# Performance work log

Measured on AMD Instinct MI355X. Metric: run time of the kernel, lower is better.

Reference implementation:

```python
import jax, jax.numpy as jnp
import numpy as np

T, B, NINP, NHID = 1024, 64, 2048, 2048


def setup_inputs() -> dict:
    key = jax.random.key(0)
    ks = jax.random.split(key, 10)
    s = 0.02  # small init for numerical sanity (torch code used uniform(0,1))
    return {
        "x": jax.random.normal(ks[0], (T, B, NINP), dtype=jnp.float32),
        "hidden": jax.random.normal(ks[1], (B, NHID), dtype=jnp.float32),
        "W_cx": jax.random.normal(ks[2], (NHID, NINP), dtype=jnp.float32) * s,
        "W_ih": jax.random.normal(ks[3], (NHID, NHID), dtype=jnp.float32) * s,
        "W_ix": jax.random.normal(ks[4], (NHID, NINP), dtype=jnp.float32) * s,
        "W_fh": jax.random.normal(ks[5], (NHID, NHID), dtype=jnp.float32) * s,
        "W_fx": jax.random.normal(ks[6], (NHID, NINP), dtype=jnp.float32) * s,
        "b_i": jnp.zeros((NHID,), dtype=jnp.float32),
        "b_f": jnp.zeros((NHID,), dtype=jnp.float32),
    }


def reference(x, hidden, W_cx, W_ih, W_ix, W_fh, W_fx, b_i, b_f):
    # Precompute all input-side projections in big batched GEMMs (same math,
    # hoisted out of the sequential loop).
    content = jnp.einsum('tbi,hi->tbh', x, W_cx)            # [T,B,H]
    ix = jnp.einsum('tbi,hi->tbh', x, W_ix) + b_i            # [T,B,H]
    fx = jnp.einsum('tbi,hi->tbh', x, W_fx) + b_f            # [T,B,H]

    def step(h, inp):
        c_t, ix_t, fx_t = inp
        i_t = jax.nn.sigmoid(h @ W_ih.T + ix_t)
        f_t = jax.nn.sigmoid(h @ W_fh.T + fx_t)
        h_new = jnp.tanh(i_t * c_t + f_t * h)
        return h_new, h_new

    nexth, output = jax.lax.scan(step, hidden, (content, ix, fx))
    return output, nexth
```

## Files before the change

### kernel.cpp

```cpp
#include <hip/hip_runtime.h>
#include <cstdint>
#include <cstddef>

#define T_SEQ 1024
#define BATCH 64
#define NH 2048

typedef _Float16 half8 __attribute__((ext_vector_type(8)));
typedef _Float16 half4 __attribute__((ext_vector_type(4)));
typedef float f32x4 __attribute__((ext_vector_type(4)));
typedef unsigned u32x4 __attribute__((ext_vector_type(4)));

__device__ inline void gload_lds16(const void* g, void* l) {
    __builtin_amdgcn_global_load_lds(
        (const __attribute__((address_space(1))) uint32_t*)g,
        (__attribute__((address_space(3))) uint32_t*)l,
        16, 0, 0);
}

#define LLC_LD16NW(dst, addr)                                                \
    asm volatile("global_load_dwordx4 %0, %1, off sc0 sc1"                   \
                 : "=v"(dst) : "v"(addr))
#define LLC_LD4(dst, addr)                                                   \
    asm volatile("global_load_dword %0, %1, off sc0 sc1\n\ts_waitcnt vmcnt(0)" \
                 : "=v"(dst) : "v"(addr))
#define LLC_LD16W(dst, addr)                                                 \
    asm volatile("global_load_dwordx4 %0, %1, off sc0 sc1\n\ts_waitcnt vmcnt(0)" \
                 : "=v"(dst) : "v"(addr))
#define LLC_ST2(addr, val)                                                   \
    asm volatile("global_store_short %0, %1, off sc0 sc1"                    \
                 :: "v"(addr), "v"(val) : "memory")
#define LLC_ST4(addr, val)                                                   \
    asm volatile("global_store_dword %0, %1, off sc0 sc1"                    \
                 :: "v"(addr), "v"(val) : "memory")
#define LLC_ST16(addr, val)                                                  \
    asm volatile("global_store_dwordx4 %0, %1, off sc0 sc1"                  \
                 :: "v"(addr), "v"(val) : "memory")

__device__ inline void wait_vm0() {
    asm volatile("s_waitcnt vmcnt(0)" ::: "memory");
}

__global__ __launch_bounds__(256) void cvt_f32_f16(const float* __restrict__ src,
                                                   _Float16* __restrict__ dst,
                                                   long long n) {
    long long i = ((long long)blockIdx.x * 256 + threadIdx.x) * 4;
    long long stride = (long long)gridDim.x * 256 * 4;
    for (; i < n; i += stride) {
        const float4 v = *(const float4*)(src + i);
        half4 o;
        o[0] = (_Float16)v.x; o[1] = (_Float16)v.y;
        o[2] = (_Float16)v.z; o[3] = (_Float16)v.w;
        *(half4*)(dst + i) = o;
    }
}

__global__ __launch_bounds__(256) void proj_gemm(const _Float16* __restrict__ A,
                                                 const _Float16* __restrict__ B,
                                                 _Float16* __restrict__ C, int M) {
    __shared__ _Float16 As[128][64];
    __shared__ _Float16 Bs[128][64];
    const int NBN = 48;
    const int nbm = M >> 7;
    const int nwg = nbm * NBN;
    const int per = nwg >> 3;
    const int bid = blockIdx.x;
    const int swz = (bid & 7) * per + (bid >> 3);
    const int bm = swz / NBN, bn = swz % NBN;

    const int tid = threadIdx.x;
    const int lane = tid & 63, w = tid >> 6;
    const int wm = w & 1, wn = w >> 1;

    f32x4 acc[4][4] = {};

    const int srow = lane >> 3;
    const int scol = (lane & 7) * 8;

    for (int bk = 0; bk < NH / 64; ++bk) {
#pragma unroll
        for (int i = 0; i < 4; ++i) {
            int r = w * 32 + i * 8;
            const _Float16* gA = A + (size_t)(bm * 128 + r + srow) * NH + bk * 64 + scol;
            gload_lds16(gA, &As[r][0]);
            const _Float16* gB = B + (size_t)(bn * 128 + r + srow) * NH + bk * 64 + scol;
            gload_lds16(gB, &Bs[r][0]);
        }
        __syncthreads();
#pragma unroll
        for (int kk = 0; kk < 2; ++kk) {
            half8 af[4], bf[4];
#pragma unroll
            for (int mi = 0; mi < 4; ++mi)
                af[mi] = *(const half8*)&As[wm * 64 + mi * 16 + (lane & 15)][kk * 32 + (lane >> 4) * 8];
#pragma unroll
            for (int ni = 0; ni < 4; ++ni)
                bf[ni] = *(const half8*)&Bs[wn * 64 + ni * 16 + (lane & 15)][kk * 32 + (lane >> 4) * 8];
#pragma unroll
            for (int mi = 0; mi < 4; ++mi)
#pragma unroll
                for (int ni = 0; ni < 4; ++ni)
                    acc[mi][ni] = __builtin_amdgcn_mfma_f32_16x16x32_f16(af[mi], bf[ni], acc[mi][ni], 0, 0, 0);
        }
        __syncthreads();
    }
#pragma unroll
    for (int mi = 0; mi < 4; ++mi)
#pragma unroll
        for (int ni = 0; ni < 4; ++ni)
#pragma unroll
            for (int r = 0; r < 4; ++r) {
                int m = bm * 128 + wm * 64 + mi * 16 + (lane >> 4) * 4 + r;
                int n = bn * 128 + wn * 64 + ni * 16 + (lane & 15);
                C[(size_t)m * 6144 + n] = (_Float16)acc[mi][ni][r];
            }
}

__global__ __launch_bounds__(512, 1) void scan_kernel(
    const _Float16* __restrict__ proj,
    const _Float16* __restrict__ Wr,
    _Float16* hb0, _Float16* hb1,
    const float* __restrict__ b_i, const float* __restrict__ b_f,
    float* __restrict__ out,
    unsigned* hflags, unsigned* pflags, float* part,
    int t0, int nsteps) {
    extern __shared__ char smem[];
    _Float16* Wlds = (_Float16*)smem;
    char* hstage = smem + 131072;

    const int wg = blockIdx.x;
    const int xcd = wg & 7;
    const int slot = wg >> 3;
    const int g = slot & 1;
    const int rem = slot >> 1;
    const int js = xcd * 4 + (rem & 3);
    const int ks = rem >> 2;
    const int j0g = js * 64;
    const int b0 = g * 32;
    const int k0 = ks * 512;

    const int tid = threadIdx.x;
    const int lane = tid & 63;
    const int w = tid >> 6;
    const int mi = w & 1;
    const int nt = w >> 1;

    unsigned* hflags_g = hflags + g * 32;
    unsigned* pflags_g = pflags + g * 128;

    for (int q = 0; q < 16; ++q) {
        int e = q * 512 + tid;
        int le = e & 63;
        int u = (e >> 6) & 15;
        int nte = (e >> 10) & 3;
        int gate = e >> 12;
        const _Float16* src = Wr + ((size_t)gate << 22) +
            (size_t)(j0g + nte * 16 + (le & 15)) * NH + k0 + u * 32 + (le >> 4) * 8;
        *(half8*)(Wlds + (((size_t)(gate * 4 + nte) * 16 + u) * 64 + le) * 8) =
            *(const half8*)src;
    }

    const int jj = j0g + nt * 16 + (lane & 15);
    const float bi_s = b_i[jj];
    const float bf_s = b_f[jj];

    float hprev[4], pc[4], pix[4], pfx[4];
    if (ks == 0) {
        const _Float16* hini = (t0 & 1) ? hb1 : hb0;
#pragma unroll
        for (int r = 0; r < 4; ++r) {
            int b = b0 + mi * 16 + (lane >> 4) * 4 + r;
            unsigned tmp;
            asm volatile("global_load_ushort %0, %1, off sc0 sc1\n\ts_waitcnt vmcnt(0)"
                         : "=v"(tmp) : "v"(hini + (size_t)b * NH + jj));
            hprev[r] = (float)__builtin_bit_cast(_Float16, (unsigned short)tmp);
            size_t pbase = (size_t)b * 6144 + jj;
            pc[r] = (float)proj[pbase];
            pix[r] = (float)proj[pbase + 2048];
            pfx[r] = (float)proj[pbase + 4096];
        }
    }

    __syncthreads();

    for (int s = 0; s < nsteps; ++s) {
        const int t = t0 + s;
        const _Float16* hcur = (t & 1) ? hb1 : hb0;
        _Float16* hnxt = (t & 1) ? hb0 : hb1;
        const unsigned tv = (unsigned)t;

        if (w == 0) {
            const unsigned* fa = hflags_g + ks * 8 + (lane & 7);
            while (true) {
                unsigned v;
                LLC_LD4(v, fa);
                if (__all((int)(v >= tv))) break;
                __builtin_amdgcn_s_sleep(1);
            }
        }
        __syncthreads();

        {
            half8 t0v, t1v, t2v, t3v;
            const _Float16* srcb = hcur + (size_t)(b0 + w * 4) * NH + k0 + lane * 8;
            LLC_LD16NW(t0v, srcb);
            LLC_LD16NW(t1v, srcb + NH);
            LLC_LD16NW(t2v, srcb + 2 * NH);
            LLC_LD16NW(t3v, srcb + 3 * NH);
            wait_vm0();
            __builtin_amdgcn_sched_barrier(0);
            const int r0 = w * 4;
            *(half8*)(hstage + (r0 + 0) * 1024 + ((lane * 16) ^ (((r0 + 0) & 7) << 4))) = t0v;
            *(half8*)(hstage + (r0 + 1) * 1024 + ((lane * 16) ^ (((r0 + 1) & 7) << 4))) = t1v;
            *(half8*)(hstage + (r0 + 2) * 1024 + ((lane * 16) ^ (((r0 + 2) & 7) << 4))) = t2v;
            *(half8*)(hstage + (r0 + 3) * 1024 + ((lane * 16) ^ (((r0 + 3) & 7) << 4))) = t3v;
        }
        __syncthreads();

        f32x4 ci = {}, cf = {};
        {
            const int arow = mi * 16 + (lane & 15);
            const char* abase = hstage + arow * 1024;
            const int axor = (arow & 7) << 4;
            const _Float16* wbi = Wlds + (((size_t)(0 * 4 + nt) * 16) * 64 + lane) * 8;
            const _Float16* wbf = Wlds + (((size_t)(1 * 4 + nt) * 16) * 64 + lane) * 8;
#pragma unroll
            for (int u = 0; u < 16; ++u) {
                half8 a = *(const half8*)(abase + ((u * 64 + (lane >> 4) * 16) ^ axor));
                half8 wi = *(const half8*)(wbi + (size_t)u * 512);
                half8 wf = *(const half8*)(wbf + (size_t)u * 512);
                ci = __builtin_amdgcn_mfma_f32_16x16x32_f16(a, wi, ci, 0, 0, 0);
                cf = __builtin_amdgcn_mfma_f32_16x16x32_f16(a, wf, cf, 0, 0, 0);
            }
        }

        if (ks != 0) {
            const int slotp = (((t & 1) * 2 + g) * 32 + js) * 3 + (ks - 1);
            float* pb = part + (size_t)slotp * 4096 + w * 512 + lane * 4;
            LLC_ST16(pb, ci);
            LLC_ST16(pb + 256, cf);
            wait_vm0();
            __syncthreads();
            if (tid == 0) LLC_ST4(pflags_g + js * 4 + (ks - 1), (unsigned)(t + 1));
        } else {
            if (w == 0) {
                const unsigned* pf = pflags_g + js * 4;
                while (true) {
                    u32x4 v;
                    LLC_LD16W(v, pf);
                    if (__all((int)(v[0] >= tv + 1 && v[1] >= tv + 1 && v[2] >= tv + 1)))
                        break;
                    __builtin_amdgcn_s_sleep(1);
                }
            }
            __syncthreads();

            f32x4 pi0, pg0, pi1, pg1, pi2, pg2;
            const int sbase = (((t & 1) * 2 + g) * 32 + js) * 3;
            const float* pb0 = part + (size_t)(sbase + 0) * 4096 + w * 512 + lane * 4;
            const float* pb1 = part + (size_t)(sbase + 1) * 4096 + w * 512 + lane * 4;
            const float* pb2 = part + (size_t)(sbase + 2) * 4096 + w * 512 + lane * 4;
            LLC_LD16NW(pi0, pb0);
            LLC_LD16NW(pg0, pb0 + 256);
            LLC_LD16NW(pi1, pb1);
            LLC_LD16NW(pg1, pb1 + 256);
            LLC_LD16NW(pi2, pb2);
            LLC_LD16NW(pg2, pb2 + 256);
            wait_vm0();
            __builtin_amdgcn_sched_barrier(0);
            ci += pi0 + pi1 + pi2;
            cf += pg0 + pg1 + pg2;

            float hn_keep[4];
#pragma unroll
            for (int r = 0; r < 4; ++r) {
                int b = b0 + mi * 16 + (lane >> 4) * 4 + r;
                float iv = 1.0f / (1.0f + __expf(-(ci[r] + pix[r] + bi_s)));
                float fv = 1.0f / (1.0f + __expf(-(cf[r] + pfx[r] + bf_s)));
                float z = iv * pc[r] + fv * hprev[r];
                float hn = 1.0f - 2.0f / (__expf(2.0f * z) + 1.0f);
                hprev[r] = hn;
                hn_keep[r] = hn;
                _Float16 hn16 = (_Float16)hn;
                LLC_ST2(hnxt + (size_t)b * NH + jj, hn16);
            }
            wait_vm0();
            __syncthreads();
            if (tid == 0) LLC_ST4(hflags_g + js, (unsigned)(t + 1));

#pragma unroll
            for (int r = 0; r < 4; ++r) {
                int b = b0 + mi * 16 + (lane >> 4) * 4 + r;
                out[(size_t)t * (BATCH * NH) + (size_t)b * NH + jj] = hn_keep[r];
                if (t == T_SEQ - 1)
                    out[(size_t)T_SEQ * (BATCH * NH) + (size_t)b * NH + jj] = hn_keep[r];
            }
            if (s + 1 < nsteps) {
#pragma unroll
                for (int r = 0; r < 4; ++r) {
                    int b = b0 + mi * 16 + (lane >> 4) * 4 + r;
                    size_t pbase = ((size_t)(s + 1) * 64 + b) * 6144 + jj;
                    pc[r] = (float)proj[pbase];
                    pix[r] = (float)proj[pbase + 2048];
                    pfx[r] = (float)proj[pbase + 4096];
                }
            }
        }
    }
}

extern "C" void kernel_launch(void* const* d_in, const int* in_sizes, int n_in,
                              void* d_out, int out_size, void* d_ws, size_t ws_size,
                              hipStream_t stream) {
    const float* x = (const float*)d_in[0];
    const float* hidden = (const float*)d_in[1];
    const float* W_cx = (const float*)d_in[2];
    const float* W_ih = (const float*)d_in[3];
    const float* W_ix = (const float*)d_in[4];
    const float* W_fh = (const float*)d_in[5];
    const float* W_fx = (const float*)d_in[6];
    const float* b_i = (const float*)d_in[7];
    const float* b_f = (const float*)d_in[8];
    float* out = (float*)d_out;

    char* ws = (char*)d_ws;
    size_t off = 0;
    auto alloc = [&](size_t bytes) {
        char* p = ws + off;
        off += (bytes + 255) & ~(size_t)255;
        return p;
    };
    _Float16* Wp = (_Float16*)alloc((size_t)6144 * NH * 2);
    _Float16* Wr = (_Float16*)alloc((size_t)2 * NH * NH * 2);
    _Float16* hb0 = (_Float16*)alloc((size_t)BATCH * NH * 2);
    _Float16* hb1 = (_Float16*)alloc((size_t)BATCH * NH * 2);
    unsigned* hflags = (unsigned*)alloc(256);
    unsigned* pflags = (unsigned*)alloc(1024);
    float* part = (float*)alloc((size_t)2 * 2 * 32 * 3 * 4096 * 4);
    const size_t fixed = off;

    int chunk = 32;
    for (int c = T_SEQ; c >= 32; c >>= 1) {
        size_t need = fixed + (size_t)c * 64 * NH * 2 + (size_t)c * 64 * 6144 * 2 + 1024;
        if (need <= ws_size) { chunk = c; break; }
    }
    _Float16* xh = (_Float16*)alloc((size_t)chunk * 64 * NH * 2);
    _Float16* proj = (_Float16*)alloc((size_t)chunk * 64 * 6144 * 2);

    hipMemsetAsync(hflags, 0, 256, stream);
    hipMemsetAsync(pflags, 0, 1024, stream);

    const long long wsz = (long long)NH * NH;
    cvt_f32_f16<<<2048, 256, 0, stream>>>(W_cx, Wp, wsz);
    cvt_f32_f16<<<2048, 256, 0, stream>>>(W_ix, Wp + wsz, wsz);
    cvt_f32_f16<<<2048, 256, 0, stream>>>(W_fx, Wp + 2 * wsz, wsz);
    cvt_f32_f16<<<2048, 256, 0, stream>>>(W_ih, Wr, wsz);
    cvt_f32_f16<<<2048, 256, 0, stream>>>(W_fh, Wr + wsz, wsz);
    cvt_f32_f16<<<128, 256, 0, stream>>>(hidden, hb0, (long long)BATCH * NH);

    const int nch = T_SEQ / chunk;
    for (int c = 0; c < nch; ++c) {
        const int t0 = c * chunk;
        const int M = chunk * 64;
        cvt_f32_f16<<<2048, 256, 0, stream>>>(x + (size_t)t0 * 64 * NH, xh, (long long)M * NH);
        proj_gemm<<<dim3((M / 128) * 48), 256, 0, stream>>>(xh, Wp, proj, M);
        scan_kernel<<<256, 512, 163840, stream>>>(proj, Wr, hb0, hb1, b_i, b_f,
                                                  out, hflags, pflags, part, t0, chunk);
    }
}
```

Measured before the change: 9.895 ms.

## Replace partial-sum flags with canary-tagged fp16 partials polled directly

The split-K partial sums exchanged between workgroups are now packed to fp16 and written as a single 16-byte store per lane. Readiness is detected by polling the data itself against an all-ones canary, which the consumer restores after reading. This removes the separate flag store, the store-side wait and __syncthreads, and the flag-poll round trip on each recurrent step, and it halves the partial traffic. In exchange the partials lose fp32 precision. Correctness depends on a 16-byte store landing atomically and on no real fp16 pair ever encoding 0xFFFFFFFF (NaN), and every wave now spins on its own data rather than one wave polling.

```diff
diff --git a/kernel.cpp b/kernel.cpp
--- a/kernel.cpp
+++ b/kernel.cpp
@@ -23,9 +23,6 @@
                  : "=v"(dst) : "v"(addr))
 #define LLC_LD4(dst, addr)                                                   \
     asm volatile("global_load_dword %0, %1, off sc0 sc1\n\ts_waitcnt vmcnt(0)" \
-                 : "=v"(dst) : "v"(addr))
-#define LLC_LD16W(dst, addr)                                                 \
-    asm volatile("global_load_dwordx4 %0, %1, off sc0 sc1\n\ts_waitcnt vmcnt(0)" \
                  : "=v"(dst) : "v"(addr))
 #define LLC_ST2(addr, val)                                                   \
     asm volatile("global_store_short %0, %1, off sc0 sc1"                    \
@@ -40,6 +37,8 @@
 __device__ inline void wait_vm0() {
     asm volatile("s_waitcnt vmcnt(0)" ::: "memory");
 }
+
+#define CANARY32 0xFFFFFFFFu
 
 __global__ __launch_bounds__(256) void cvt_f32_f16(const float* __restrict__ src,
                                                    _Float16* __restrict__ dst,
@@ -122,7 +121,7 @@
     _Float16* hb0, _Float16* hb1,
     const float* __restrict__ b_i, const float* __restrict__ b_f,
     float* __restrict__ out,
-    unsigned* hflags, unsigned* pflags, float* part,
+    unsigned* hflags, _Float16* part,
     int t0, int nsteps) {
     extern __shared__ char smem[];
     _Float16* Wlds = (_Float16*)smem;
@@ -146,7 +145,6 @@
     const int nt = w >> 1;
 
     unsigned* hflags_g = hflags + g * 32;
-    unsigned* pflags_g = pflags + g * 128;
 
     for (int q = 0; q < 16; ++q) {
         int e = q * 512 + tid;
@@ -234,42 +232,47 @@
             }
         }
 
+        const size_t tilebase = (size_t)(((t & 1) * 2 + g) * 32 + js) * 3;
+
         if (ks != 0) {
-            const int slotp = (((t & 1) * 2 + g) * 32 + js) * 3 + (ks - 1);
-            float* pb = part + (size_t)slotp * 4096 + w * 512 + lane * 4;
-            LLC_ST16(pb, ci);
-            LLC_ST16(pb + 256, cf);
-            wait_vm0();
-            __syncthreads();
-            if (tid == 0) LLC_ST4(pflags_g + js * 4 + (ks - 1), (unsigned)(t + 1));
+            half8 pk;
+#pragma unroll
+            for (int r = 0; r < 4; ++r) {
+                pk[r] = (_Float16)ci[r];
+                pk[4 + r] = (_Float16)cf[r];
+            }
+            _Float16* pb = part + ((tilebase + (ks - 1)) * 8 + w) * 512 + lane * 8;
+            LLC_ST16(pb, pk);
         } else {
-            if (w == 0) {
-                const unsigned* pf = pflags_g + js * 4;
-                while (true) {
-                    u32x4 v;
-                    LLC_LD16W(v, pf);
-                    if (__all((int)(v[0] >= tv + 1 && v[1] >= tv + 1 && v[2] >= tv + 1)))
-                        break;
-                    __builtin_amdgcn_s_sleep(1);
-                }
-            }
-            __syncthreads();
-
-            f32x4 pi0, pg0, pi1, pg1, pi2, pg2;
-            const int sbase = (((t & 1) * 2 + g) * 32 + js) * 3;
-            const float* pb0 = part + (size_t)(sbase + 0) * 4096 + w * 512 + lane * 4;
-            const float* pb1 = part + (size_t)(sbase + 1) * 4096 + w * 512 + lane * 4;
-            const float* pb2 = part + (size_t)(sbase + 2) * 4096 + w * 512 + lane * 4;
-            LLC_LD16NW(pi0, pb0);
-            LLC_LD16NW(pg0, pb0 + 256);
-            LLC_LD16NW(pi1, pb1);
-            LLC_LD16NW(pg1, pb1 + 256);
-            LLC_LD16NW(pi2, pb2);
-            LLC_LD16NW(pg2, pb2 + 256);
-            wait_vm0();
+            _Float16* s0 = part + ((tilebase + 0) * 8 + w) * 512 + lane * 8;
+            _Float16* s1 = part + ((tilebase + 1) * 8 + w) * 512 + lane * 8;
+            _Float16* s2 = part + ((tilebase + 2) * 8 + w) * 512 + lane * 8;
+            u32x4 q0, q1, q2;
+            while (true) {
+                LLC_LD16NW(q0, s0);
+                LLC_LD16NW(q1, s1);
+                LLC_LD16NW(q2, s2);
+                wait_vm0();
+                __builtin_amdgcn_sched_barrier(0);
+                bool ok = (q0[0] != CANARY32) && (q1[0] != CANARY32) && (q2[0] != CANARY32);
+                if (__all(ok)) break;
+                __builtin_amdgcn_s_sleep(1);
+            }
             __builtin_amdgcn_sched_barrier(0);
-            ci += pi0 + pi1 + pi2;
-            cf += pg0 + pg1 + pg2;
+            u32x4 can;
+            can[0] = CANARY32; can[1] = CANARY32; can[2] = CANARY32; can[3] = CANARY32;
+            LLC_ST16(s0, can);
+            LLC_ST16(s1, can);
+            LLC_ST16(s2, can);
+
+            half8 p0 = __builtin_bit_cast(half8, q0);
+            half8 p1 = __builtin_bit_cast(half8, q1);
+            half8 p2 = __builtin_bit_cast(half8, q2);
+#pragma unroll
+            for (int r = 0; r < 4; ++r) {
+                ci[r] += (float)p0[r] + (float)p1[r] + (float)p2[r];
+                cf[r] += (float)p0[4 + r] + (float)p1[4 + r] + (float)p2[4 + r];
+            }
 
             float hn_keep[4];
 #pragma unroll
@@ -335,8 +338,8 @@
     _Float16* hb0 = (_Float16*)alloc((size_t)BATCH * NH * 2);
     _Float16* hb1 = (_Float16*)alloc((size_t)BATCH * NH * 2);
     unsigned* hflags = (unsigned*)alloc(256);
-    unsigned* pflags = (unsigned*)alloc(1024);
-    float* part = (float*)alloc((size_t)2 * 2 * 32 * 3 * 4096 * 4);
+    const size_t part_bytes = (size_t)2 * 2 * 32 * 3 * 8 * 512 * 2;
+    _Float16* part = (_Float16*)alloc(part_bytes);
     const size_t fixed = off;
 
     int chunk = 32;
@@ -348,7 +351,7 @@
     _Float16* proj = (_Float16*)alloc((size_t)chunk * 64 * 6144 * 2);
 
     hipMemsetAsync(hflags, 0, 256, stream);
-    hipMemsetAsync(pflags, 0, 1024, stream);
+    hipMemsetAsync(part, 0xFF, part_bytes, stream);
 
     const long long wsz = (long long)NH * NH;
     cvt_f32_f16<<<2048, 256, 0, stream>>>(W_cx, Wp, wsz);
@@ -365,6 +368,6 @@
         cvt_f32_f16<<<2048, 256, 0, stream>>>(x + (size_t)t0 * 64 * NH, xh, (long long)M * NH);
         proj_gemm<<<dim3((M / 128) * 48), 256, 0, stream>>>(xh, Wp, proj, M);
         scan_kernel<<<256, 512, 163840, stream>>>(proj, Wr, hb0, hb1, b_i, b_f,
-                                                  out, hflags, pflags, part, t0, chunk);
-    }
-}
+                                                  out, hflags, part, t0, chunk);
+    }
+}
```

Result: no change. 9.870 ms (-0.2%).
